# Kernel tuning notes

Hardware: AMD Instinct MI355X
Metric: run time of the kernel (lower is better)

The kernel has to match this reference:

```python
import jax, jax.numpy as jnp
import numpy as np

B, S, C = 8, 1024, 1280   # B = 2*N (uncond|cond halves), S = 32*32 latent tokens
H, D = 20, 64             # heads, head_dim; H*D == C


def setup_inputs() -> dict:
    key = jax.random.key(0)
    ks = jax.random.split(key, 5)
    std = 1.0 / np.sqrt(C)
    return {
        "hidden_states": jax.random.normal(ks[0], (B, S, C), jnp.float32),
        "Wq": jax.random.normal(ks[1], (C, C), jnp.float32) * std,
        "Wk": jax.random.normal(ks[2], (C, C), jnp.float32) * std,
        "Wv": jax.random.normal(ks[3], (C, C), jnp.float32) * std,
        "Wo": jax.random.normal(ks[4], (C, C), jnp.float32) * std,
        "bo": jnp.zeros((C,), jnp.float32),
    }


def _inject(x, n):
    # replicate reference rows 0 (uncond) and n (cond) across each half
    unc = jnp.broadcast_to(x[0:1], (n,) + x.shape[1:])
    con = jnp.broadcast_to(x[n:n + 1], (n,) + x.shape[1:])
    return jnp.concatenate([unc, con], axis=0)


def reference(hidden_states, Wq, Wk, Wv, Wo, bo):
    b, s, c = hidden_states.shape
    n = b // 2
    q = hidden_states @ Wq
    k = hidden_states @ Wk
    v = hidden_states @ Wv
    # PnP injection (self-attention, share_enabled, n > 1, all injections on)
    q = _inject(q, n)
    k = _inject(k, n)
    v = _inject(v, n)
    # head split: [b, s, c] -> [b, h, s, d]
    q = q.reshape(b, s, H, D).transpose(0, 2, 1, 3)
    k = k.reshape(b, s, H, D).transpose(0, 2, 1, 3)
    v = v.reshape(b, s, H, D).transpose(0, 2, 1, 3)
    scale = 1.0 / np.sqrt(D)
    scores = jnp.einsum("bhqd,bhkd->bhqk", q, k) * scale
    probs = jax.nn.softmax(scores, axis=-1)
    out = jnp.einsum("bhqk,bhkd->bhqd", probs, v)
    out = out.transpose(0, 2, 1, 3).reshape(b, s, c)
    return out @ Wo + bo
```

## Files before the change

### kernel.cpp

```cpp
#include <hip/hip_runtime.h>

#define S_LEN 1024
#define C_DIM 1280
#define NH 20
#define HD 64

typedef __attribute__((ext_vector_type(8))) short short8;
typedef __attribute__((ext_vector_type(4))) short short4v;
typedef __attribute__((ext_vector_type(4))) float float4v;

__device__ __forceinline__ float bf2f(unsigned short u) {
    union { unsigned u; float f; } v; v.u = ((unsigned)u) << 16; return v.f;
}
__device__ __forceinline__ unsigned short f2bf(float f) {
    union { float f; unsigned u; } v; v.f = f;
    unsigned u = v.u;
    return (unsigned short)((u + 0x7FFFu + ((u >> 16) & 1u)) >> 16);
}

__device__ __forceinline__ void load_lds16(const unsigned short* g, unsigned short* l) {
    __builtin_amdgcn_global_load_lds(
        (const __attribute__((address_space(1))) unsigned int*)g,
        (__attribute__((address_space(3))) unsigned int*)l, 16, 0, 0);
}

__global__ __launch_bounds__(256) void detect_kernel(
    const unsigned int* __restrict__ w, int* __restrict__ flag)
{
    __shared__ int cnt;
    if (threadIdx.x == 0) cnt = 0;
    __syncthreads();
    int local = 0;
    for (int i = threadIdx.x; i < 1024; i += 256) {
        unsigned e = (w[i] >> 7) & 0xFFu;
        if (e >= 100u && e <= 140u) local++;
    }
    atomicAdd(&cnt, local);
    __syncthreads();
    if (threadIdx.x == 0) *flag = (cnt < 512) ? 1 : 0;
}

__global__ __launch_bounds__(256) void convx_kernel(
    const void* __restrict__ hs, const int* __restrict__ flag,
    unsigned short* __restrict__ X)
{
    const size_t SC = (size_t)S_LEN * C_DIM;
    int g = blockIdx.y;
    size_t off = ((size_t)blockIdx.x * 256 + threadIdx.x) * 8;
    size_t src = (size_t)g * 4 * SC + off;
    short8 o;
    if (*flag) {
        const float* p = (const float*)hs + src;
        for (int j = 0; j < 8; j++) o[j] = (short)f2bf(p[j]);
    } else {
        o = *(const short8*)((const unsigned short*)hs + src);
    }
    *(short8*)(X + g * SC + off) = o;
}

__global__ __launch_bounds__(256) void convw_kernel(
    const void* __restrict__ Wq, const void* __restrict__ Wk,
    const void* __restrict__ Wv, const void* __restrict__ Wo,
    const int* __restrict__ flag, unsigned short* __restrict__ WT)
{
    __shared__ unsigned short tile[64 * 68];
    const void* W = (blockIdx.z == 0) ? Wq : (blockIdx.z == 1) ? Wk
                    : (blockIdx.z == 2) ? Wv : Wo;
    unsigned short* T = WT + (size_t)blockIdx.z * C_DIM * C_DIM;
    int fp32 = *flag;
    int c0 = blockIdx.x * 64, r0 = blockIdx.y * 64;
    int t = threadIdx.x;
    int r = t >> 3, cg = t & 7;
    for (int rep = 0; rep < 2; rep++) {
        int rr = r0 + r + rep * 32;
        if (fp32) {
            const float* p = (const float*)W + (size_t)rr * C_DIM + c0 + cg * 8;
            for (int j = 0; j < 8; j++)
                tile[(r + rep * 32) * 68 + cg * 8 + j] = f2bf(p[j]);
        } else {
            short8 v = *(const short8*)((const unsigned short*)W + (size_t)rr * C_DIM + c0 + cg * 8);
            for (int j = 0; j < 8; j++)
                tile[(r + rep * 32) * 68 + cg * 8 + j] = (unsigned short)v[j];
        }
    }
    __syncthreads();
    int c = t >> 3, rg = t & 7;
    for (int rep = 0; rep < 2; rep++) {
        short8 o;
        for (int j = 0; j < 8; j++)
            o[j] = (short)tile[(rg * 8 + j) * 68 + c + rep * 32];
        *(short8*)(T + (size_t)(c0 + c + rep * 32) * C_DIM + r0 + rg * 8) = o;
    }
}

__global__ __launch_bounds__(256) void gemm_qkv_kernel(
    const unsigned short* __restrict__ X,
    const unsigned short* __restrict__ WT,
    unsigned short* __restrict__ Qo, unsigned short* __restrict__ Ko,
    unsigned short* __restrict__ Vt)
{
    __shared__ __align__(16) unsigned short Al[2][128 * 64];
    __shared__ __align__(16) unsigned short Bl[2][128 * 64];
    int z = blockIdx.z;
    const unsigned short* Wt = WT + (size_t)z * C_DIM * C_DIM;
    int c0 = blockIdx.x * 128, r0 = blockIdx.y * 128;
    int t = threadIdx.x, wave = t >> 6, lane = t & 63;
    int wr = wave >> 1, wc = wave & 1, quad = lane >> 4, mn = lane & 15;
    int srow = wave * 8 + (lane >> 3), slot = lane & 7;
    const unsigned short* xb = X + (size_t)r0 * C_DIM;
    const unsigned short* wb = Wt + (size_t)c0 * C_DIM;

    auto stage = [&](int ki, int buf) {
        int k0 = ki * 64;
        for (int p = 0; p < 4; p++) {
            int row = p * 32 + srow; int ck = slot ^ (row & 7);
            load_lds16(xb + (size_t)row * C_DIM + k0 + ck * 8, &Al[buf][row * 64 + slot * 8]);
        }
        for (int p = 0; p < 4; p++) {
            int row = p * 32 + srow; int ck = slot ^ (row & 7);
            load_lds16(wb + (size_t)row * C_DIM + k0 + ck * 8, &Bl[buf][row * 64 + slot * 8]);
        }
    };

    stage(0, 0);
    asm volatile("s_waitcnt vmcnt(0)" ::: "memory");
    __builtin_amdgcn_s_barrier();

    float4v acc[4][4] = {};
    for (int kt = 0; kt < 20; kt++) {
        int cur = kt & 1, nxt = cur ^ 1;
        if (kt < 19) stage(kt + 1, nxt);
        for (int kc = 0; kc < 2; kc++) {
            short8 a[4], b[4];
            for (int mt = 0; mt < 4; mt++) {
                int row = wr * 64 + mt * 16 + mn;
                a[mt] = *(const short8*)(&Al[cur][row * 64 + (((kc * 4 + quad) ^ (row & 7)) * 8)]);
            }
            for (int nt = 0; nt < 4; nt++) {
                int row = wc * 64 + nt * 16 + mn;
                b[nt] = *(const short8*)(&Bl[cur][row * 64 + (((kc * 4 + quad) ^ (row & 7)) * 8)]);
            }
            for (int mt = 0; mt < 4; mt++)
                for (int nt = 0; nt < 4; nt++)
                    acc[mt][nt] = __builtin_amdgcn_mfma_f32_16x16x32_bf16(a[mt], b[nt], acc[mt][nt], 0, 0, 0);
        }
        asm volatile("s_waitcnt vmcnt(0)" ::: "memory");
        __builtin_amdgcn_s_barrier();
    }

    if (z == 2) {
        int g = r0 >> 10;
        for (int mt = 0; mt < 4; mt++) {
            int row = r0 + wr * 64 + mt * 16 + quad * 4;
            int s = row & 1023;
            for (int nt = 0; nt < 4; nt++) {
                int col = c0 + wc * 64 + nt * 16 + mn;
                short4v p;
                for (int i = 0; i < 4; i++) p[i] = (short)f2bf(acc[mt][nt][i]);
                *(short4v*)(Vt + ((size_t)g * C_DIM + col) * S_LEN + s) = p;
            }
        }
    } else {
        unsigned short* Out = (z == 0) ? Qo : Ko;
        for (int mt = 0; mt < 4; mt++) {
            int row = r0 + wr * 64 + mt * 16 + quad * 4;
            for (int nt = 0; nt < 4; nt++) {
                int col = c0 + wc * 64 + nt * 16 + mn;
                for (int i = 0; i < 4; i++)
                    Out[(size_t)(row + i) * C_DIM + col] = f2bf(acc[mt][nt][i]);
            }
        }
    }
}

__global__ __launch_bounds__(256) void attn_kernel(
    const unsigned short* __restrict__ Q, const unsigned short* __restrict__ K,
    const unsigned short* __restrict__ VT, unsigned short* __restrict__ O)
{
    __shared__ __align__(16) unsigned short Kl[2][64 * 64];
    __shared__ __align__(16) unsigned short Vl[2][64 * 64];
    __shared__ unsigned short Pl[4 * 16 * 72];
    int qt = blockIdx.x, h = blockIdx.y, g = blockIdx.z;
    int t = threadIdx.x, wave = t >> 6, lane = t & 63;
    int quad = lane >> 4, n = lane & 15;
    const size_t SC = (size_t)S_LEN * C_DIM;
    const unsigned short* Qb = Q + (size_t)g * SC;
    const unsigned short* Kb = K + (size_t)g * SC + h * HD;
    const unsigned short* Vb = VT + (size_t)g * SC + (size_t)(h * HD) * S_LEN;
    unsigned short* Pw = &Pl[wave * 16 * 72];

    int srow = wave * 8 + (lane >> 3);
    int slot = lane & 7;

    short8 qa[2];
    int qrow = qt * 64 + wave * 16 + n;
    for (int kc = 0; kc < 2; kc++) {
        short8 v = *(const short8*)(Qb + (size_t)qrow * C_DIM + h * HD + kc * 32 + quad * 8);
        short8 w;
        for (int j = 0; j < 8; j++)
            w[j] = (short)f2bf(bf2f((unsigned short)v[j]) * 0.125f);
        qa[kc] = w;
    }

    for (int p = 0; p < 2; p++) {
        int row = p * 32 + srow;
        int ck = slot ^ (row & 7);
        load_lds16(Kb + (size_t)row * C_DIM + ck * 8, &Kl[0][row * 64 + slot * 8]);
        load_lds16(Vb + (size_t)row * S_LEN + ck * 8, &Vl[0][row * 64 + slot * 8]);
    }
    asm volatile("s_waitcnt vmcnt(0)" ::: "memory");
    __builtin_amdgcn_s_barrier();

    float4v oacc[4] = {};
    float lsum[4] = { 0.f, 0.f, 0.f, 0.f };

    for (int kt = 0; kt < 16; kt++) {
        int cur = kt & 1, nxt = cur ^ 1;
        if (kt < 15) {
            for (int p = 0; p < 2; p++) {
                int row = p * 32 + srow;
                int ck = slot ^ (row & 7);
                load_lds16(Kb + (size_t)((kt + 1) * 64 + row) * C_DIM + ck * 8,
                           &Kl[nxt][row * 64 + slot * 8]);
                load_lds16(Vb + (size_t)row * S_LEN + (kt + 1) * 64 + ck * 8,
                           &Vl[nxt][row * 64 + slot * 8]);
            }
        }
        const unsigned short* Kt = Kl[cur];
        const unsigned short* Vt = Vl[cur];

        float4v sacc[4] = {};
        for (int kc = 0; kc < 2; kc++)
            for (int nt = 0; nt < 4; nt++) {
                int row = nt * 16 + n;
                short8 kb = *(const short8*)(Kt + row * 64 + (((kc * 4 + quad) ^ (row & 7)) * 8));
                sacc[nt] = __builtin_amdgcn_mfma_f32_16x16x32_bf16(qa[kc], kb, sacc[nt], 0, 0, 0);
            }

        for (int nt = 0; nt < 4; nt++)
            for (int i = 0; i < 4; i++) {
                float p = __expf(sacc[nt][i]);
                lsum[i] += p;
                Pw[(quad * 4 + i) * 72 + nt * 16 + n] = f2bf(p);
            }
        asm volatile("s_waitcnt lgkmcnt(0)" ::: "memory");
        short8 pa0 = *(const short8*)(&Pw[n * 72 + quad * 8]);
        short8 pa1 = *(const short8*)(&Pw[n * 72 + 32 + quad * 8]);
        for (int kc = 0; kc < 2; kc++) {
            short8 pa = kc ? pa1 : pa0;
            for (int nt = 0; nt < 4; nt++) {
                int row = nt * 16 + n;
                short8 vb = *(const short8*)(Vt + row * 64 + (((kc * 4 + quad) ^ (row & 7)) * 8));
                oacc[nt] = __builtin_amdgcn_mfma_f32_16x16x32_bf16(pa, vb, oacc[nt], 0, 0, 0);
            }
        }
        asm volatile("s_waitcnt vmcnt(0)" ::: "memory");
        __builtin_amdgcn_s_barrier();
    }

    for (int i = 0; i < 4; i++)
        for (int d = 1; d < 16; d <<= 1)
            lsum[i] += __shfl_xor(lsum[i], d, 64);
    float inv[4];
    for (int i = 0; i < 4; i++) inv[i] = 1.0f / lsum[i];

    int row0 = qt * 64 + wave * 16 + quad * 4;
    for (int nt = 0; nt < 4; nt++)
        for (int i = 0; i < 4; i++)
            O[(size_t)g * SC + (size_t)(row0 + i) * C_DIM + h * HD + nt * 16 + n] =
                f2bf(oacc[nt][i] * inv[i]);
}

__global__ __launch_bounds__(256) void gemm_out_kernel(
    const unsigned short* __restrict__ X,
    const unsigned short* __restrict__ WoT,
    const void* __restrict__ bo,
    const int* __restrict__ flag,
    void* __restrict__ out)
{
    __shared__ __align__(16) unsigned short Al[2][64 * 64];
    __shared__ __align__(16) unsigned short Bl[2][64 * 64];
    int c0 = blockIdx.x * 64, r0 = blockIdx.y * 64;
    int t = threadIdx.x, wave = t >> 6, lane = t & 63;
    int wr = wave >> 1, wc = wave & 1, quad = lane >> 4, mn = lane & 15;
    int srow = wave * 8 + (lane >> 3), slot = lane & 7;
    const unsigned short* xb = X + (size_t)r0 * C_DIM;
    const unsigned short* wb = WoT + (size_t)c0 * C_DIM;
    int fp32 = *flag;

    for (int p = 0; p < 2; p++) {
        int row = p * 32 + srow; int ck = slot ^ (row & 7);
        load_lds16(xb + (size_t)row * C_DIM + ck * 8, &Al[0][row * 64 + slot * 8]);
        load_lds16(wb + (size_t)row * C_DIM + ck * 8, &Bl[0][row * 64 + slot * 8]);
    }
    asm volatile("s_waitcnt vmcnt(0)" ::: "memory");
    __builtin_amdgcn_s_barrier();

    float4v acc[2][2] = {};
    for (int kt = 0; kt < 20; kt++) {
        int cur = kt & 1, nxt = cur ^ 1;
        if (kt < 19) {
            int k0 = (kt + 1) * 64;
            for (int p = 0; p < 2; p++) {
                int row = p * 32 + srow; int ck = slot ^ (row & 7);
                load_lds16(xb + (size_t)row * C_DIM + k0 + ck * 8, &Al[nxt][row * 64 + slot * 8]);
                load_lds16(wb + (size_t)row * C_DIM + k0 + ck * 8, &Bl[nxt][row * 64 + slot * 8]);
            }
        }
        for (int kc = 0; kc < 2; kc++) {
            short8 a[2], b[2];
            for (int mt = 0; mt < 2; mt++) {
                int row = wr * 32 + mt * 16 + mn;
                a[mt] = *(const short8*)(&Al[cur][row * 64 + (((kc * 4 + quad) ^ (row & 7)) * 8)]);
            }
            for (int nt = 0; nt < 2; nt++) {
                int row = wc * 32 + nt * 16 + mn;
                b[nt] = *(const short8*)(&Bl[cur][row * 64 + (((kc * 4 + quad) ^ (row & 7)) * 8)]);
            }
            for (int mt = 0; mt < 2; mt++)
                for (int nt = 0; nt < 2; nt++)
                    acc[mt][nt] = __builtin_amdgcn_mfma_f32_16x16x32_bf16(a[mt], b[nt], acc[mt][nt], 0, 0, 0);
        }
        asm volatile("s_waitcnt vmcnt(0)" ::: "memory");
        __builtin_amdgcn_s_barrier();
    }

    for (int mt = 0; mt < 2; mt++) {
        int row = r0 + wr * 32 + mt * 16 + quad * 4;
        int g = row >> 10;
        for (int nt = 0; nt < 2; nt++) {
            int col = c0 + wc * 32 + nt * 16 + mn;
            float bb = fp32 ? ((const float*)bo)[col] : bf2f(((const unsigned short*)bo)[col]);
            for (int i = 0; i < 4; i++) {
                float v = acc[mt][nt][i] + bb;
                int s = (row + i) & 1023;
                if (fp32) {
                    float* o = (float*)out;
                    for (int rep = 0; rep < 4; rep++)
                        o[((size_t)(g * 4 + rep) * S_LEN + s) * C_DIM + col] = v;
                } else {
                    unsigned short* o = (unsigned short*)out;
                    unsigned short bv = f2bf(v);
                    for (int rep = 0; rep < 4; rep++)
                        o[((size_t)(g * 4 + rep) * S_LEN + s) * C_DIM + col] = bv;
                }
            }
        }
    }
}

extern "C" void kernel_launch(void* const* d_in, const int* in_sizes, int n_in,
                              void* d_out, int out_size, void* d_ws, size_t ws_size,
                              hipStream_t stream)
{
    const void* hs = d_in[0];
    const void* Wq = d_in[1];
    const void* Wk = d_in[2];
    const void* Wv = d_in[3];
    const void* Wo = d_in[4];
    const void* bo = d_in[5];

    const size_t CC  = (size_t)C_DIM * C_DIM;
    const size_t SC2 = (size_t)2 * S_LEN * C_DIM;

    int* flag = (int*)d_ws;
    unsigned short* base = (unsigned short*)((char*)d_ws + 256);
    unsigned short* WT = base;
    unsigned short* X  = WT + 4 * CC;
    unsigned short* Q  = X + SC2;
    unsigned short* K  = Q + SC2;
    unsigned short* VT = K + SC2;

    hipLaunchKernelGGL(detect_kernel, dim3(1), dim3(256), 0, stream,
                       (const unsigned int*)Wq, flag);
    hipLaunchKernelGGL(convx_kernel, dim3(640, 2), dim3(256), 0, stream,
                       hs, flag, X);
    hipLaunchKernelGGL(convw_kernel, dim3(20, 20, 4), dim3(256), 0, stream,
                       Wq, Wk, Wv, Wo, flag, WT);
    hipLaunchKernelGGL(gemm_qkv_kernel, dim3(10, 16, 3), dim3(256), 0, stream,
                       X, WT, Q, K, VT);
    hipLaunchKernelGGL(attn_kernel, dim3(16, NH, 2), dim3(256), 0, stream,
                       Q, K, VT, X );
    hipLaunchKernelGGL(gemm_out_kernel, dim3(20, 32), dim3(256), 0, stream,
                       X, WT + 3 * CC, bo, flag, d_out);
}
```

Measured before the change: 207.1 us.

## Remap block indices for XCD locality and enlarge attention and output GEMM tiles

The QKV GEMM, attention and output GEMM launches become 1D grids with custom index remapping. The intent is to group blocks that share operands onto the same XCD (the remap uses lin&7) and to balance the tail. Attention blocks now process 128 query rows (two 64-row sub-tiles per wave), so each K/V tile loaded into LDS is reused twice. The output GEMM moves to 64x128 tiles, giving 320 blocks instead of 640. Fewer blocks means less parallelism and more registers and LDS per block, which could hurt occupancy.

```diff
diff --git a/kernel.cpp b/kernel.cpp
--- a/kernel.cpp
+++ b/kernel.cpp
@@ -101,9 +101,19 @@
 {
     __shared__ __align__(16) unsigned short Al[2][128 * 64];
     __shared__ __align__(16) unsigned short Bl[2][128 * 64];
-    int z = blockIdx.z;
+    int lin = blockIdx.x;
+    int r = lin & 7, j = lin >> 3;
+    int pl = j >> 4, y = j & 15;
+    int p = pl * 8 + r;
+    if (p >= 30) {
+        int idx = (r - 6) * 12 + (j - 48);
+        p = 24 + (idx >> 2);
+        y = 12 + (idx & 3);
+    }
+    int x = p % 10, z = p / 10;
+    int c0 = x * 128, r0 = y * 128;
+
     const unsigned short* Wt = WT + (size_t)z * C_DIM * C_DIM;
-    int c0 = blockIdx.x * 128, r0 = blockIdx.y * 128;
     int t = threadIdx.x, wave = t >> 6, lane = t & 63;
     int wr = wave >> 1, wc = wave & 1, quad = lane >> 4, mn = lane & 15;
     int srow = wave * 8 + (lane >> 3), slot = lane & 7;
@@ -112,12 +122,12 @@
 
     auto stage = [&](int ki, int buf) {
         int k0 = ki * 64;
-        for (int p = 0; p < 4; p++) {
-            int row = p * 32 + srow; int ck = slot ^ (row & 7);
+        for (int q = 0; q < 4; q++) {
+            int row = q * 32 + srow; int ck = slot ^ (row & 7);
             load_lds16(xb + (size_t)row * C_DIM + k0 + ck * 8, &Al[buf][row * 64 + slot * 8]);
         }
-        for (int p = 0; p < 4; p++) {
-            int row = p * 32 + srow; int ck = slot ^ (row & 7);
+        for (int q = 0; q < 4; q++) {
+            int row = q * 32 + srow; int ck = slot ^ (row & 7);
             load_lds16(wb + (size_t)row * C_DIM + k0 + ck * 8, &Bl[buf][row * 64 + slot * 8]);
         }
     };
@@ -155,9 +165,9 @@
             int s = row & 1023;
             for (int nt = 0; nt < 4; nt++) {
                 int col = c0 + wc * 64 + nt * 16 + mn;
-                short4v p;
-                for (int i = 0; i < 4; i++) p[i] = (short)f2bf(acc[mt][nt][i]);
-                *(short4v*)(Vt + ((size_t)g * C_DIM + col) * S_LEN + s) = p;
+                short4v pk;
+                for (int i = 0; i < 4; i++) pk[i] = (short)f2bf(acc[mt][nt][i]);
+                *(short4v*)(Vt + ((size_t)g * C_DIM + col) * S_LEN + s) = pk;
             }
         }
     } else {
@@ -179,31 +189,37 @@
 {
     __shared__ __align__(16) unsigned short Kl[2][64 * 64];
     __shared__ __align__(16) unsigned short Vl[2][64 * 64];
-    __shared__ unsigned short Pl[4 * 16 * 72];
-    int qt = blockIdx.x, h = blockIdx.y, g = blockIdx.z;
+    __shared__ unsigned short Pl[8][16 * 72];
+    int lin = blockIdx.x;
+    int r = lin & 7, j = lin >> 3;
+    int pair = (j >> 3) * 8 + r;
+    int qt = j & 7;
+    int h = pair % 20, g = pair / 20;
+
     int t = threadIdx.x, wave = t >> 6, lane = t & 63;
     int quad = lane >> 4, n = lane & 15;
     const size_t SC = (size_t)S_LEN * C_DIM;
     const unsigned short* Qb = Q + (size_t)g * SC;
     const unsigned short* Kb = K + (size_t)g * SC + h * HD;
     const unsigned short* Vb = VT + (size_t)g * SC + (size_t)(h * HD) * S_LEN;
-    unsigned short* Pw = &Pl[wave * 16 * 72];
 
     int srow = wave * 8 + (lane >> 3);
     int slot = lane & 7;
 
-    short8 qa[2];
-    int qrow = qt * 64 + wave * 16 + n;
-    for (int kc = 0; kc < 2; kc++) {
-        short8 v = *(const short8*)(Qb + (size_t)qrow * C_DIM + h * HD + kc * 32 + quad * 8);
-        short8 w;
-        for (int j = 0; j < 8; j++)
-            w[j] = (short)f2bf(bf2f((unsigned short)v[j]) * 0.125f);
-        qa[kc] = w;
-    }
-
-    for (int p = 0; p < 2; p++) {
-        int row = p * 32 + srow;
+    short8 qa[2][2];
+    for (int a = 0; a < 2; a++) {
+        int qrow = qt * 128 + a * 64 + wave * 16 + n;
+        for (int kc = 0; kc < 2; kc++) {
+            short8 v = *(const short8*)(Qb + (size_t)qrow * C_DIM + h * HD + kc * 32 + quad * 8);
+            short8 w;
+            for (int jj = 0; jj < 8; jj++)
+                w[jj] = (short)f2bf(bf2f((unsigned short)v[jj]) * 0.125f);
+            qa[a][kc] = w;
+        }
+    }
+
+    for (int q = 0; q < 2; q++) {
+        int row = q * 32 + srow;
         int ck = slot ^ (row & 7);
         load_lds16(Kb + (size_t)row * C_DIM + ck * 8, &Kl[0][row * 64 + slot * 8]);
         load_lds16(Vb + (size_t)row * S_LEN + ck * 8, &Vl[0][row * 64 + slot * 8]);
@@ -211,14 +227,14 @@
     asm volatile("s_waitcnt vmcnt(0)" ::: "memory");
     __builtin_amdgcn_s_barrier();
 
-    float4v oacc[4] = {};
-    float lsum[4] = { 0.f, 0.f, 0.f, 0.f };
+    float4v oacc[2][4] = {};
+    float lsum[2][4] = {};
 
     for (int kt = 0; kt < 16; kt++) {
         int cur = kt & 1, nxt = cur ^ 1;
         if (kt < 15) {
-            for (int p = 0; p < 2; p++) {
-                int row = p * 32 + srow;
+            for (int q = 0; q < 2; q++) {
+                int row = q * 32 + srow;
                 int ck = slot ^ (row & 7);
                 load_lds16(Kb + (size_t)((kt + 1) * 64 + row) * C_DIM + ck * 8,
                            &Kl[nxt][row * 64 + slot * 8]);
@@ -229,46 +245,51 @@
         const unsigned short* Kt = Kl[cur];
         const unsigned short* Vt = Vl[cur];
 
-        float4v sacc[4] = {};
+        float4v sacc[2][4] = {};
         for (int kc = 0; kc < 2; kc++)
             for (int nt = 0; nt < 4; nt++) {
                 int row = nt * 16 + n;
                 short8 kb = *(const short8*)(Kt + row * 64 + (((kc * 4 + quad) ^ (row & 7)) * 8));
-                sacc[nt] = __builtin_amdgcn_mfma_f32_16x16x32_bf16(qa[kc], kb, sacc[nt], 0, 0, 0);
-            }
-
-        for (int nt = 0; nt < 4; nt++)
-            for (int i = 0; i < 4; i++) {
-                float p = __expf(sacc[nt][i]);
-                lsum[i] += p;
-                Pw[(quad * 4 + i) * 72 + nt * 16 + n] = f2bf(p);
-            }
+                for (int a = 0; a < 2; a++)
+                    sacc[a][nt] = __builtin_amdgcn_mfma_f32_16x16x32_bf16(qa[a][kc], kb, sacc[a][nt], 0, 0, 0);
+            }
+
+        for (int a = 0; a < 2; a++)
+            for (int nt = 0; nt < 4; nt++)
+                for (int i = 0; i < 4; i++) {
+                    float pv = __expf(sacc[a][nt][i]);
+                    lsum[a][i] += pv;
+                    Pl[wave * 2 + a][(quad * 4 + i) * 72 + nt * 16 + n] = f2bf(pv);
+                }
         asm volatile("s_waitcnt lgkmcnt(0)" ::: "memory");
-        short8 pa0 = *(const short8*)(&Pw[n * 72 + quad * 8]);
-        short8 pa1 = *(const short8*)(&Pw[n * 72 + 32 + quad * 8]);
-        for (int kc = 0; kc < 2; kc++) {
-            short8 pa = kc ? pa1 : pa0;
+        short8 pa[2][2];
+        for (int a = 0; a < 2; a++) {
+            pa[a][0] = *(const short8*)(&Pl[wave * 2 + a][n * 72 + quad * 8]);
+            pa[a][1] = *(const short8*)(&Pl[wave * 2 + a][n * 72 + 32 + quad * 8]);
+        }
+        for (int kc = 0; kc < 2; kc++)
             for (int nt = 0; nt < 4; nt++) {
                 int row = nt * 16 + n;
                 short8 vb = *(const short8*)(Vt + row * 64 + (((kc * 4 + quad) ^ (row & 7)) * 8));
-                oacc[nt] = __builtin_amdgcn_mfma_f32_16x16x32_bf16(pa, vb, oacc[nt], 0, 0, 0);
-            }
-        }
+                for (int a = 0; a < 2; a++)
+                    oacc[a][nt] = __builtin_amdgcn_mfma_f32_16x16x32_bf16(pa[a][kc], vb, oacc[a][nt], 0, 0, 0);
+            }
         asm volatile("s_waitcnt vmcnt(0)" ::: "memory");
         __builtin_amdgcn_s_barrier();
     }
 
-    for (int i = 0; i < 4; i++)
-        for (int d = 1; d < 16; d <<= 1)
-            lsum[i] += __shfl_xor(lsum[i], d, 64);
-    float inv[4];
-    for (int i = 0; i < 4; i++) inv[i] = 1.0f / lsum[i];
-
-    int row0 = qt * 64 + wave * 16 + quad * 4;
-    for (int nt = 0; nt < 4; nt++)
+    for (int a = 0; a < 2; a++) {
         for (int i = 0; i < 4; i++)
-            O[(size_t)g * SC + (size_t)(row0 + i) * C_DIM + h * HD + nt * 16 + n] =
-                f2bf(oacc[nt][i] * inv[i]);
+            for (int d = 1; d < 16; d <<= 1)
+                lsum[a][i] += __shfl_xor(lsum[a][i], d, 64);
+        float inv[4];
+        for (int i = 0; i < 4; i++) inv[i] = 1.0f / lsum[a][i];
+        int row0 = qt * 128 + a * 64 + wave * 16 + quad * 4;
+        for (int nt = 0; nt < 4; nt++)
+            for (int i = 0; i < 4; i++)
+                O[(size_t)g * SC + (size_t)(row0 + i) * C_DIM + h * HD + nt * 16 + n] =
+                    f2bf(oacc[a][nt][i] * inv[i]);
+    }
 }
 
 __global__ __launch_bounds__(256) void gemm_out_kernel(
@@ -279,45 +300,51 @@
     void* __restrict__ out)
 {
     __shared__ __align__(16) unsigned short Al[2][64 * 64];
-    __shared__ __align__(16) unsigned short Bl[2][64 * 64];
-    int c0 = blockIdx.x * 64, r0 = blockIdx.y * 64;
+    __shared__ __align__(16) unsigned short Bl[2][128 * 64];
+    int lin = blockIdx.x;
+    int x, y;
+    if (lin < 256) { x = lin & 7; y = lin >> 3; }
+    else           { x = 8 + ((lin - 256) >> 5); y = (lin - 256) & 31; }
+    int c0 = x * 128, r0 = y * 64;
+
     int t = threadIdx.x, wave = t >> 6, lane = t & 63;
-    int wr = wave >> 1, wc = wave & 1, quad = lane >> 4, mn = lane & 15;
+    int quad = lane >> 4, mn = lane & 15;
     int srow = wave * 8 + (lane >> 3), slot = lane & 7;
     const unsigned short* xb = X + (size_t)r0 * C_DIM;
     const unsigned short* wb = WoT + (size_t)c0 * C_DIM;
     int fp32 = *flag;
 
-    for (int p = 0; p < 2; p++) {
-        int row = p * 32 + srow; int ck = slot ^ (row & 7);
-        load_lds16(xb + (size_t)row * C_DIM + ck * 8, &Al[0][row * 64 + slot * 8]);
-        load_lds16(wb + (size_t)row * C_DIM + ck * 8, &Bl[0][row * 64 + slot * 8]);
-    }
+    auto stage = [&](int ki, int buf) {
+        int k0 = ki * 64;
+        for (int q = 0; q < 2; q++) {
+            int row = q * 32 + srow; int ck = slot ^ (row & 7);
+            load_lds16(xb + (size_t)row * C_DIM + k0 + ck * 8, &Al[buf][row * 64 + slot * 8]);
+        }
+        for (int q = 0; q < 4; q++) {
+            int row = q * 32 + srow; int ck = slot ^ (row & 7);
+            load_lds16(wb + (size_t)row * C_DIM + k0 + ck * 8, &Bl[buf][row * 64 + slot * 8]);
+        }
+    };
+
+    stage(0, 0);
     asm volatile("s_waitcnt vmcnt(0)" ::: "memory");
     __builtin_amdgcn_s_barrier();
 
-    float4v acc[2][2] = {};
+    float4v acc[4][2] = {};
     for (int kt = 0; kt < 20; kt++) {
         int cur = kt & 1, nxt = cur ^ 1;
-        if (kt < 19) {
-            int k0 = (kt + 1) * 64;
-            for (int p = 0; p < 2; p++) {
-                int row = p * 32 + srow; int ck = slot ^ (row & 7);
-                load_lds16(xb + (size_t)row * C_DIM + k0 + ck * 8, &Al[nxt][row * 64 + slot * 8]);
-                load_lds16(wb + (size_t)row * C_DIM + k0 + ck * 8, &Bl[nxt][row * 64 + slot * 8]);
-            }
-        }
+        if (kt < 19) stage(kt + 1, nxt);
         for (int kc = 0; kc < 2; kc++) {
-            short8 a[2], b[2];
-            for (int mt = 0; mt < 2; mt++) {
-                int row = wr * 32 + mt * 16 + mn;
+            short8 a[4], b[2];
+            for (int mt = 0; mt < 4; mt++) {
+                int row = mt * 16 + mn;
                 a[mt] = *(const short8*)(&Al[cur][row * 64 + (((kc * 4 + quad) ^ (row & 7)) * 8)]);
             }
             for (int nt = 0; nt < 2; nt++) {
-                int row = wc * 32 + nt * 16 + mn;
+                int row = wave * 32 + nt * 16 + mn;
                 b[nt] = *(const short8*)(&Bl[cur][row * 64 + (((kc * 4 + quad) ^ (row & 7)) * 8)]);
             }
-            for (int mt = 0; mt < 2; mt++)
+            for (int mt = 0; mt < 4; mt++)
                 for (int nt = 0; nt < 2; nt++)
                     acc[mt][nt] = __builtin_amdgcn_mfma_f32_16x16x32_bf16(a[mt], b[nt], acc[mt][nt], 0, 0, 0);
         }
@@ -325,11 +352,11 @@
         __builtin_amdgcn_s_barrier();
     }
 
-    for (int mt = 0; mt < 2; mt++) {
-        int row = r0 + wr * 32 + mt * 16 + quad * 4;
+    for (int mt = 0; mt < 4; mt++) {
+        int row = r0 + mt * 16 + quad * 4;
         int g = row >> 10;
         for (int nt = 0; nt < 2; nt++) {
-            int col = c0 + wc * 32 + nt * 16 + mn;
+            int col = c0 + wave * 32 + nt * 16 + mn;
             float bb = fp32 ? ((const float*)bo)[col] : bf2f(((const unsigned short*)bo)[col]);
             for (int i = 0; i < 4; i++) {
                 float v = acc[mt][nt][i] + bb;
@@ -377,10 +404,10 @@
                        hs, flag, X);
     hipLaunchKernelGGL(convw_kernel, dim3(20, 20, 4), dim3(256), 0, stream,
                        Wq, Wk, Wv, Wo, flag, WT);
-    hipLaunchKernelGGL(gemm_qkv_kernel, dim3(10, 16, 3), dim3(256), 0, stream,
+    hipLaunchKernelGGL(gemm_qkv_kernel, dim3(480), dim3(256), 0, stream,
                        X, WT, Q, K, VT);
-    hipLaunchKernelGGL(attn_kernel, dim3(16, NH, 2), dim3(256), 0, stream,
+    hipLaunchKernelGGL(attn_kernel, dim3(320), dim3(256), 0, stream,
                        Q, K, VT, X );
-    hipLaunchKernelGGL(gemm_out_kernel, dim3(20, 32), dim3(256), 0, stream,
+    hipLaunchKernelGGL(gemm_out_kernel, dim3(320), dim3(256), 0, stream,
                        X, WT + 3 * CC, bo, flag, d_out);
 }
```

New measurement: 212.6 us. +2.6%, slower.
